# Kernel optimization log

Measured on AMD Instinct MI355X. Metric: run time of the kernel, lower is better.

The kernel has to match this reference:

```python
import jax, jax.numpy as jnp
import numpy as np

N, E, D, H, C = 20000, 320000, 256, 8, 32
NEG_SLOPE = 0.2


def setup_inputs() -> dict:
    key = jax.random.key(0)
    ks = jax.random.split(key, 9)
    s = 1.0 / np.sqrt(D)
    x = jax.random.normal(ks[0], (N, D), dtype=jnp.float32)
    edge_index = jax.random.randint(ks[1], (2, E), 0, N, dtype=jnp.int32)
    # positive edge weights in (0.05, 1.0] so log() is finite
    edge_attr = jax.random.uniform(ks[2], (E,), dtype=jnp.float32, minval=0.05, maxval=1.0)
    W_l = jax.random.normal(ks[3], (D, H * C), dtype=jnp.float32) * s
    b_l = jax.random.normal(ks[4], (H * C,), dtype=jnp.float32) * 0.01
    W_r = jax.random.normal(ks[5], (D, H * C), dtype=jnp.float32) * s
    b_r = jax.random.normal(ks[6], (H * C,), dtype=jnp.float32) * 0.01
    att = jax.random.normal(ks[7], (H, C), dtype=jnp.float32) * (1.0 / np.sqrt(C))
    bias = jax.random.normal(ks[8], (H * C,), dtype=jnp.float32) * 0.01
    return {"x": x, "edge_index": edge_index, "edge_attr": edge_attr,
            "W_l": W_l, "b_l": b_l, "W_r": W_r, "b_r": b_r,
            "att": att, "bias": bias}


def reference(x, edge_index, edge_attr, W_l, b_l, W_r, b_r, att, bias):
    n = x.shape[0]
    # GATv2: separate linear transforms for source (l) and target (r) nodes
    x_l = (x @ W_l + b_l).reshape(n, H, C)  # source / x_j
    x_r = (x @ W_r + b_r).reshape(n, H, C)  # target / x_i
    src, dst = edge_index[0], edge_index[1]  # flow: source_to_target, index = dst

    x_j = x_l[src]                            # [E, H, C]
    g = jax.nn.leaky_relu(x_r[dst] + x_j, NEG_SLOPE)
    alpha = jnp.einsum('ehc,hc->eh', g, att)  # [E, H]
    alpha = alpha + jnp.log(edge_attr)[:, None]

    # segment softmax over destination node (ragged edge groups)
    amax = jax.ops.segment_max(alpha, dst, num_segments=n)  # [N, H]
    ex = jnp.exp(alpha - amax[dst])
    denom = jax.ops.segment_sum(ex, dst, num_segments=n)
    alpha = ex / (denom[dst] + 1e-16)

    # message = x_j * alpha, scatter-add into destination nodes
    out = jax.ops.segment_sum(x_j * alpha[..., None], dst, num_segments=n)  # [N, H, C]
    return out.reshape(n, H * C) + bias
```

## Files before the change

### kernel.cpp

```cpp
#include <hip/hip_runtime.h>
#include <hip/hip_bf16.h>
#include <math.h>

#define DD 256
#define NHEAD 8
#define NEG_SLOPE 0.2f
#define CAP 64

typedef __attribute__((ext_vector_type(16))) float f32x16;
typedef __attribute__((ext_vector_type(8)))  short bf16x8;
typedef _Float16 h2 __attribute__((ext_vector_type(2)));

union Frag { bf16x8 v; uint4 u4; };
union HU4  { uint4 u4; h2 h[4]; };

__device__ inline uint f2bf(float f) {
    __hip_bfloat16 h = __float2bfloat16(f);
    return (uint)*(ushort*)&h;
}
__device__ inline ushort f2h(float f) {
    _Float16 h = (_Float16)f;
    return *(ushort*)&h;
}
__device__ inline h2 pkmax(h2 a, h2 b) {
    h2 d;
    asm("v_pk_max_f16 %0, %1, %2" : "=v"(d) : "v"(a), "v"(b));
    return d;
}
__device__ inline float hdot2(h2 a, h2 b, float c) {
#if __has_builtin(__builtin_amdgcn_fdot2)
    return __builtin_amdgcn_fdot2(a, b, c, false);
#else
    return c + (float)a.x * (float)b.x + (float)a.y * (float)b.y;
#endif
}

__global__ __launch_bounds__(256) void prep_kernel(const float* __restrict__ x,
                                                   const float* __restrict__ Wl,
                                                   const float* __restrict__ Wr,
                                                   ushort* __restrict__ pa,
                                                   ushort* __restrict__ pw,
                                                   int* __restrict__ counts,
                                                   int N, int Mpad) {
    int idx = blockIdx.x * 256 + threadIdx.x;
    if (idx < N) { counts[idx] = 0; return; }
    idx -= N;
    const int na = Mpad * 32;
    if (idx < na) {
        int lane = idx & 63;
        int mi   = (idx >> 6) & 1;
        int s16  = (idx >> 7) & 15;
        int tile = idx >> 11;
        int m = tile * 64 + mi * 32 + (lane & 31);
        int g = lane >> 5;
        uint4 val = {0u, 0u, 0u, 0u};
        if (m < N) {
            const float* xp = x + (size_t)m * DD + s16 * 16 + g * 4;
            float4 f0 = *(const float4*)xp;
            float4 f1 = *(const float4*)(xp + 8);
            val.x = f2bf(f0.x) | (f2bf(f0.y) << 16);
            val.y = f2bf(f0.z) | (f2bf(f0.w) << 16);
            val.z = f2bf(f1.x) | (f2bf(f1.y) << 16);
            val.w = f2bf(f1.z) | (f2bf(f1.w) << 16);
        }
        *(uint4*)(pa + (size_t)idx * 8) = val;
        return;
    }
    idx -= na;
    if (idx < 16384) {
        int lane = idx & 63;
        int s16  = (idx >> 6) & 15;
        int ng   = (idx >> 10) & 7;
        int mat  = idx >> 13;
        const float* W = mat ? Wr : Wl;
        int n  = ng * 32 + (lane & 31);
        int k0 = s16 * 16 + (lane >> 5) * 4;
        uint4 val;
        val.x = f2bf(W[(size_t)(k0 + 0) * DD + n]) | (f2bf(W[(size_t)(k0 + 1) * DD + n]) << 16);
        val.y = f2bf(W[(size_t)(k0 + 2) * DD + n]) | (f2bf(W[(size_t)(k0 + 3) * DD + n]) << 16);
        val.z = f2bf(W[(size_t)(k0 + 8) * DD + n]) | (f2bf(W[(size_t)(k0 + 9) * DD + n]) << 16);
        val.w = f2bf(W[(size_t)(k0 +10) * DD + n]) | (f2bf(W[(size_t)(k0 +11) * DD + n]) << 16);
        *(uint4*)(pw + (size_t)idx * 8) = val;
    }
}

__global__ __launch_bounds__(256) void scatter_kernel(const int* __restrict__ src,
                                                      const int* __restrict__ dst,
                                                      const float* __restrict__ w,
                                                      int* __restrict__ counts,
                                                      int2* __restrict__ csr_sw,
                                                      int E) {
    int e = blockIdx.x * 256 + threadIdx.x;
    if (e < E) {
        int d = dst[e];
        int pos = atomicAdd(&counts[d], 1);
        if (pos < CAP)
            csr_sw[((size_t)d << 6) + pos] = make_int2(src[e], __float_as_int(w[e]));
    }
}

__global__ __launch_bounds__(256, 4) void mm_kernel(const ushort* __restrict__ pa,
                                                    const ushort* __restrict__ pw,
                                                    const float* __restrict__ bl,
                                                    const float* __restrict__ br,
                                                    ushort* __restrict__ xl_h,
                                                    ushort* __restrict__ xr_h,
                                                    int N) {
    const int t    = threadIdx.x;
    const int lane = t & 63;
    const int l31  = lane & 31;
    const int g    = lane >> 5;
    const int wd   = t >> 6;
    const int tile = blockIdx.x, mat = blockIdx.y;

    const ushort* paT = pa + (size_t)tile * 2048 * 8;
    const ushort* pb  = pw + ((size_t)mat * 8192 + (size_t)(2 * wd) * 1024) * 8;

    f32x16 acc00, acc01, acc10, acc11;
    #pragma unroll
    for (int i = 0; i < 16; ++i) { acc00[i] = 0.f; acc01[i] = 0.f; acc10[i] = 0.f; acc11[i] = 0.f; }

    #pragma unroll 4
    for (int s16 = 0; s16 < 16; ++s16) {
        Frag a0, a1, b0, b1;
        a0.u4 = *(const uint4*)(paT + (size_t)((s16 * 2 + 0) * 64 + lane) * 8);
        a1.u4 = *(const uint4*)(paT + (size_t)((s16 * 2 + 1) * 64 + lane) * 8);
        b0.u4 = *(const uint4*)(pb  + (size_t)((s16     ) * 64 + lane) * 8);
        b1.u4 = *(const uint4*)(pb  + (size_t)((16 + s16) * 64 + lane) * 8);
        acc00 = __builtin_amdgcn_mfma_f32_32x32x16_bf16(a0.v, b0.v, acc00, 0, 0, 0);
        acc01 = __builtin_amdgcn_mfma_f32_32x32x16_bf16(a0.v, b1.v, acc01, 0, 0, 0);
        acc10 = __builtin_amdgcn_mfma_f32_32x32x16_bf16(a1.v, b0.v, acc10, 0, 0, 0);
        acc11 = __builtin_amdgcn_mfma_f32_32x32x16_bf16(a1.v, b1.v, acc11, 0, 0, 0);
    }

    const int n0 = wd * 64 + l31;
    const int n1 = n0 + 32;
    const float* bp = (mat == 0) ? bl : br;
    const float bv0 = bp[n0], bv1 = bp[n1];
    const int mb = tile * 64;
    ushort* dstp = (mat == 0) ? xl_h : xr_h;
    #pragma unroll
    for (int r = 0; r < 16; ++r) {
        int mloc = (r & 3) + 8 * (r >> 2) + 4 * g;
        int m0 = mb + mloc, m1 = m0 + 32;
        if (m0 < N) {
            dstp[(size_t)m0 * DD + n0] = f2h(acc00[r] + bv0);
            dstp[(size_t)m0 * DD + n1] = f2h(acc01[r] + bv1);
        }
        if (m1 < N) {
            dstp[(size_t)m1 * DD + n0] = f2h(acc10[r] + bv0);
            dstp[(size_t)m1 * DD + n1] = f2h(acc11[r] + bv1);
        }
    }
}

__global__ __launch_bounds__(256) void node_kernel(const int* __restrict__ counts,
                                                   const int2* __restrict__ csr_sw,
                                                   const ushort* __restrict__ xl_h,
                                                   const ushort* __restrict__ xr_h,
                                                   const float* __restrict__ att,
                                                   const float* __restrict__ bias,
                                                   float* __restrict__ out,
                                                   int N) {
    const int wid  = threadIdx.x >> 6;
    const int lane = threadIdx.x & 63;
    const int d = blockIdx.x * 4 + wid;
    if (d >= N) return;
    const int l31 = lane & 31;
    const int hi  = lane >> 5;
    const int c0  = l31 * 8;

    const size_t beg = (size_t)d << 6;
    const int deg = min(counts[d], CAP);

    HU4 xru; xru.u4 = *(const uint4*)(xr_h + (size_t)d * DD + c0);
    const float4 af0 = *(const float4*)(att + c0);
    const float4 af1 = *(const float4*)(att + c0 + 4);
    const h2 at0 = {(_Float16)af0.x, (_Float16)af0.y};
    const h2 at1 = {(_Float16)af0.z, (_Float16)af0.w};
    const h2 at2 = {(_Float16)af1.x, (_Float16)af1.y};
    const h2 at3 = {(_Float16)af1.z, (_Float16)af1.w};
    const h2 slope = {(_Float16)NEG_SLOPE, (_Float16)NEG_SLOPE};

    float dsum = 0.f;
    float ac[8];
    #pragma unroll
    for (int j = 0; j < 8; ++j) ac[j] = 0.f;

    auto body = [&](const HU4& xv, float we) {
        h2 a0 = xv.h[0] + xru.h[0];
        h2 a1 = xv.h[1] + xru.h[1];
        h2 a2 = xv.h[2] + xru.h[2];
        h2 a3 = xv.h[3] + xru.h[3];
        h2 g0 = pkmax(a0, a0 * slope);
        h2 g1 = pkmax(a1, a1 * slope);
        h2 g2 = pkmax(a2, a2 * slope);
        h2 g3 = pkmax(a3, a3 * slope);
        float p = hdot2(g3, at3, hdot2(g2, at2, hdot2(g1, at1, hdot2(g0, at0, 0.f))));
        p += __shfl_xor(p, 1);
        p += __shfl_xor(p, 2);
        float ev = we * __expf(p);
        dsum += ev;
        ac[0] += ev * (float)xv.h[0].x;
        ac[1] += ev * (float)xv.h[0].y;
        ac[2] += ev * (float)xv.h[1].x;
        ac[3] += ev * (float)xv.h[1].y;
        ac[4] += ev * (float)xv.h[2].x;
        ac[5] += ev * (float)xv.h[2].y;
        ac[6] += ev * (float)xv.h[3].x;
        ac[7] += ev * (float)xv.h[3].y;
    };

    const int npair = (deg + 1) >> 1;
    const int dm1   = deg - 1;
    int i = 0;
    for (; i + 2 <= npair; i += 2) {
        const int iA = 2 * i + hi;
        const int iB = iA + 2;
        int2 swA = csr_sw[beg + min(iA, dm1)];
        int2 swB = csr_sw[beg + min(iB, dm1)];
        float wA = (iA < deg) ? __int_as_float(swA.y) : 0.f;
        float wB = (iB < deg) ? __int_as_float(swB.y) : 0.f;
        HU4 xvA; xvA.u4 = *(const uint4*)(xl_h + (size_t)swA.x * DD + c0);
        HU4 xvB; xvB.u4 = *(const uint4*)(xl_h + (size_t)swB.x * DD + c0);
        body(xvA, wA);
        body(xvB, wB);
    }
    if (i < npair) {
        const int iA = 2 * i + hi;
        int2 swA = csr_sw[beg + min(iA, dm1)];
        float wA = (iA < deg) ? __int_as_float(swA.y) : 0.f;
        HU4 xvA; xvA.u4 = *(const uint4*)(xl_h + (size_t)swA.x * DD + c0);
        body(xvA, wA);
    }

    dsum += __shfl_xor(dsum, 32);
    #pragma unroll
    for (int j = 0; j < 8; ++j) ac[j] += __shfl_xor(ac[j], 32);
    const float inv = 1.f / (dsum + 1e-16f);

    const float4 bv = *(const float4*)(bias + c0 + 4 * hi);
    const int b = 4 * hi;
    float4 o;
    o.x = ac[b + 0] * inv + bv.x;
    o.y = ac[b + 1] * inv + bv.y;
    o.z = ac[b + 2] * inv + bv.z;
    o.w = ac[b + 3] * inv + bv.w;
    *(float4*)(out + (size_t)d * DD + c0 + 4 * hi) = o;
}

extern "C" void kernel_launch(void* const* d_in, const int* in_sizes, int n_in,
                              void* d_out, int out_size, void* d_ws, size_t ws_size,
                              hipStream_t stream) {
    const float* x    = (const float*)d_in[0];
    const int*   ei   = (const int*)  d_in[1];
    const float* w    = (const float*)d_in[2];
    const float* Wl   = (const float*)d_in[3];
    const float* bl   = (const float*)d_in[4];
    const float* Wr   = (const float*)d_in[5];
    const float* br   = (const float*)d_in[6];
    const float* att  = (const float*)d_in[7];
    const float* bias = (const float*)d_in[8];

    const int N = in_sizes[0] / DD;
    const int E = in_sizes[2];
    const int* src = ei;
    const int* dst = ei + E;

    const int Mtiles = (N + 63) / 64;
    const int Mpad   = Mtiles * 64;

    ushort* xr_h    = (ushort*)d_ws;
    ushort* xl_h    = xr_h + (size_t)N * DD;
    ushort* pa      = xl_h + (size_t)N * DD;
    ushort* pw      = pa + (size_t)Mpad * DD;
    int2*   csr_sw  = (int2*)(pw + 131072);
    int*    counts  = (int*)(csr_sw + (size_t)N * CAP);

    float* out = (float*)d_out;

    const int prep_total = N + Mpad * 32 + 16384;
    prep_kernel   <<<(prep_total + 255) / 256, 256, 0, stream>>>(x, Wl, Wr,
                                                                 pa, pw, counts,
                                                                 N, Mpad);
    scatter_kernel<<<(E + 255) / 256, 256, 0, stream>>>(src, dst, w, counts,
                                                        csr_sw, E);
    mm_kernel     <<<dim3(Mtiles, 2), 256, 0, stream>>>(pa, pw, bl, br,
                                                        xl_h, xr_h, N);
    node_kernel   <<<(N + 3) / 4, 256, 0, stream>>>(counts, csr_sw,
                                                    xl_h, xr_h, att, bias, out, N);
}
```

Before: 77.19 us.

## Fuse x bf16 conversion into matmul, use fp16 accumulators, unroll gather by four

Removes the packed-A staging pass from the prep kernel: the matmul now reads fp32 rows of x directly and converts them to bf16 in registers before the MFMA. This drops a full write and reread of the packed activation buffer, but each of the two matrix blocks now reads x in fp32. The node kernel keeps its weighted feature sums in packed fp16 and unrolls the edge gather loop by four, putting more loads in flight. The fp16 accumulation risks precision loss and overflow on high-degree nodes.

```diff
diff --git a/kernel.cpp b/kernel.cpp
--- a/kernel.cpp
+++ b/kernel.cpp
@@ -34,39 +34,23 @@
     return c + (float)a.x * (float)b.x + (float)a.y * (float)b.y;
 #endif
 }
-
-__global__ __launch_bounds__(256) void prep_kernel(const float* __restrict__ x,
-                                                   const float* __restrict__ Wl,
+__device__ inline uint4 pack8bf(float4 lo, float4 hi) {
+    uint4 v;
+    v.x = f2bf(lo.x) | (f2bf(lo.y) << 16);
+    v.y = f2bf(lo.z) | (f2bf(lo.w) << 16);
+    v.z = f2bf(hi.x) | (f2bf(hi.y) << 16);
+    v.w = f2bf(hi.z) | (f2bf(hi.w) << 16);
+    return v;
+}
+
+__global__ __launch_bounds__(256) void prep_kernel(const float* __restrict__ Wl,
                                                    const float* __restrict__ Wr,
-                                                   ushort* __restrict__ pa,
                                                    ushort* __restrict__ pw,
                                                    int* __restrict__ counts,
-                                                   int N, int Mpad) {
+                                                   int N) {
     int idx = blockIdx.x * 256 + threadIdx.x;
     if (idx < N) { counts[idx] = 0; return; }
     idx -= N;
-    const int na = Mpad * 32;
-    if (idx < na) {
-        int lane = idx & 63;
-        int mi   = (idx >> 6) & 1;
-        int s16  = (idx >> 7) & 15;
-        int tile = idx >> 11;
-        int m = tile * 64 + mi * 32 + (lane & 31);
-        int g = lane >> 5;
-        uint4 val = {0u, 0u, 0u, 0u};
-        if (m < N) {
-            const float* xp = x + (size_t)m * DD + s16 * 16 + g * 4;
-            float4 f0 = *(const float4*)xp;
-            float4 f1 = *(const float4*)(xp + 8);
-            val.x = f2bf(f0.x) | (f2bf(f0.y) << 16);
-            val.y = f2bf(f0.z) | (f2bf(f0.w) << 16);
-            val.z = f2bf(f1.x) | (f2bf(f1.y) << 16);
-            val.w = f2bf(f1.z) | (f2bf(f1.w) << 16);
-        }
-        *(uint4*)(pa + (size_t)idx * 8) = val;
-        return;
-    }
-    idx -= na;
     if (idx < 16384) {
         int lane = idx & 63;
         int s16  = (idx >> 6) & 15;
@@ -99,7 +83,7 @@
     }
 }
 
-__global__ __launch_bounds__(256, 4) void mm_kernel(const ushort* __restrict__ pa,
+__global__ __launch_bounds__(256, 4) void mm_kernel(const float* __restrict__ x,
                                                     const ushort* __restrict__ pw,
                                                     const float* __restrict__ bl,
                                                     const float* __restrict__ br,
@@ -112,9 +96,11 @@
     const int g    = lane >> 5;
     const int wd   = t >> 6;
     const int tile = blockIdx.x, mat = blockIdx.y;
-
-    const ushort* paT = pa + (size_t)tile * 2048 * 8;
-    const ushort* pb  = pw + ((size_t)mat * 8192 + (size_t)(2 * wd) * 1024) * 8;
+    const int mb   = tile * 64;
+
+    const float* xrow0 = x + (size_t)min(mb + l31,      N - 1) * DD;
+    const float* xrow1 = x + (size_t)min(mb + 32 + l31, N - 1) * DD;
+    const ushort* pb   = pw + ((size_t)mat * 8192 + (size_t)(2 * wd) * 1024) * 8;
 
     f32x16 acc00, acc01, acc10, acc11;
     #pragma unroll
@@ -122,11 +108,16 @@
 
     #pragma unroll 4
     for (int s16 = 0; s16 < 16; ++s16) {
+        const int off = s16 * 16 + g * 4;
         Frag a0, a1, b0, b1;
-        a0.u4 = *(const uint4*)(paT + (size_t)((s16 * 2 + 0) * 64 + lane) * 8);
-        a1.u4 = *(const uint4*)(paT + (size_t)((s16 * 2 + 1) * 64 + lane) * 8);
-        b0.u4 = *(const uint4*)(pb  + (size_t)((s16     ) * 64 + lane) * 8);
-        b1.u4 = *(const uint4*)(pb  + (size_t)((16 + s16) * 64 + lane) * 8);
+        float4 lo0 = *(const float4*)(xrow0 + off);
+        float4 hi0 = *(const float4*)(xrow0 + off + 8);
+        float4 lo1 = *(const float4*)(xrow1 + off);
+        float4 hi1 = *(const float4*)(xrow1 + off + 8);
+        b0.u4 = *(const uint4*)(pb + (size_t)((s16     ) * 64 + lane) * 8);
+        b1.u4 = *(const uint4*)(pb + (size_t)((16 + s16) * 64 + lane) * 8);
+        a0.u4 = pack8bf(lo0, hi0);
+        a1.u4 = pack8bf(lo1, hi1);
         acc00 = __builtin_amdgcn_mfma_f32_32x32x16_bf16(a0.v, b0.v, acc00, 0, 0, 0);
         acc01 = __builtin_amdgcn_mfma_f32_32x32x16_bf16(a0.v, b1.v, acc01, 0, 0, 0);
         acc10 = __builtin_amdgcn_mfma_f32_32x32x16_bf16(a1.v, b0.v, acc10, 0, 0, 0);
@@ -137,7 +128,6 @@
     const int n1 = n0 + 32;
     const float* bp = (mat == 0) ? bl : br;
     const float bv0 = bp[n0], bv1 = bp[n1];
-    const int mb = tile * 64;
     ushort* dstp = (mat == 0) ? xl_h : xr_h;
     #pragma unroll
     for (int r = 0; r < 16; ++r) {
@@ -183,9 +173,9 @@
     const h2 slope = {(_Float16)NEG_SLOPE, (_Float16)NEG_SLOPE};
 
     float dsum = 0.f;
-    float ac[8];
-    #pragma unroll
-    for (int j = 0; j < 8; ++j) ac[j] = 0.f;
+    h2 ac2[4];
+    #pragma unroll
+    for (int j = 0; j < 4; ++j) ac2[j] = (h2){(_Float16)0.f, (_Float16)0.f};
 
     auto body = [&](const HU4& xv, float we) {
         h2 a0 = xv.h[0] + xru.h[0];
@@ -201,32 +191,38 @@
         p += __shfl_xor(p, 2);
         float ev = we * __expf(p);
         dsum += ev;
-        ac[0] += ev * (float)xv.h[0].x;
-        ac[1] += ev * (float)xv.h[0].y;
-        ac[2] += ev * (float)xv.h[1].x;
-        ac[3] += ev * (float)xv.h[1].y;
-        ac[4] += ev * (float)xv.h[2].x;
-        ac[5] += ev * (float)xv.h[2].y;
-        ac[6] += ev * (float)xv.h[3].x;
-        ac[7] += ev * (float)xv.h[3].y;
+        _Float16 evh = (_Float16)ev;
+        h2 evv = {evh, evh};
+        ac2[0] += evv * xv.h[0];
+        ac2[1] += evv * xv.h[1];
+        ac2[2] += evv * xv.h[2];
+        ac2[3] += evv * xv.h[3];
     };
 
     const int npair = (deg + 1) >> 1;
     const int dm1   = deg - 1;
     int i = 0;
-    for (; i + 2 <= npair; i += 2) {
+    for (; i + 4 <= npair; i += 4) {
         const int iA = 2 * i + hi;
-        const int iB = iA + 2;
+        const int iB = iA + 2, iC = iA + 4, iD = iA + 6;
         int2 swA = csr_sw[beg + min(iA, dm1)];
         int2 swB = csr_sw[beg + min(iB, dm1)];
+        int2 swC = csr_sw[beg + min(iC, dm1)];
+        int2 swD = csr_sw[beg + min(iD, dm1)];
         float wA = (iA < deg) ? __int_as_float(swA.y) : 0.f;
         float wB = (iB < deg) ? __int_as_float(swB.y) : 0.f;
+        float wC = (iC < deg) ? __int_as_float(swC.y) : 0.f;
+        float wD = (iD < deg) ? __int_as_float(swD.y) : 0.f;
         HU4 xvA; xvA.u4 = *(const uint4*)(xl_h + (size_t)swA.x * DD + c0);
         HU4 xvB; xvB.u4 = *(const uint4*)(xl_h + (size_t)swB.x * DD + c0);
+        HU4 xvC; xvC.u4 = *(const uint4*)(xl_h + (size_t)swC.x * DD + c0);
+        HU4 xvD; xvD.u4 = *(const uint4*)(xl_h + (size_t)swD.x * DD + c0);
         body(xvA, wA);
         body(xvB, wB);
-    }
-    if (i < npair) {
+        body(xvC, wC);
+        body(xvD, wD);
+    }
+    for (; i < npair; ++i) {
         const int iA = 2 * i + hi;
         int2 swA = csr_sw[beg + min(iA, dm1)];
         float wA = (iA < deg) ? __int_as_float(swA.y) : 0.f;
@@ -234,6 +230,12 @@
         body(xvA, wA);
     }
 
+    float ac[8];
+    #pragma unroll
+    for (int j = 0; j < 4; ++j) {
+        ac[2 * j]     = (float)ac2[j].x;
+        ac[2 * j + 1] = (float)ac2[j].y;
+    }
     dsum += __shfl_xor(dsum, 32);
     #pragma unroll
     for (int j = 0; j < 8; ++j) ac[j] += __shfl_xor(ac[j], 32);
@@ -268,24 +270,21 @@
     const int* dst = ei + E;
 
     const int Mtiles = (N + 63) / 64;
-    const int Mpad   = Mtiles * 64;
 
     ushort* xr_h    = (ushort*)d_ws;
     ushort* xl_h    = xr_h + (size_t)N * DD;
-    ushort* pa      = xl_h + (size_t)N * DD;
-    ushort* pw      = pa + (size_t)Mpad * DD;
+    ushort* pw      = xl_h + (size_t)N * DD;
     int2*   csr_sw  = (int2*)(pw + 131072);
     int*    counts  = (int*)(csr_sw + (size_t)N * CAP);
 
     float* out = (float*)d_out;
 
-    const int prep_total = N + Mpad * 32 + 16384;
-    prep_kernel   <<<(prep_total + 255) / 256, 256, 0, stream>>>(x, Wl, Wr,
-                                                                 pa, pw, counts,
-                                                                 N, Mpad);
+    const int prep_total = N + 16384;
+    prep_kernel   <<<(prep_total + 255) / 256, 256, 0, stream>>>(Wl, Wr, pw,
+                                                                 counts, N);
     scatter_kernel<<<(E + 255) / 256, 256, 0, stream>>>(src, dst, w, counts,
                                                         csr_sw, E);
-    mm_kernel     <<<dim3(Mtiles, 2), 256, 0, stream>>>(pa, pw, bl, br,
+    mm_kernel     <<<dim3(Mtiles, 2), 256, 0, stream>>>(x, pw, bl, br,
                                                         xl_h, xr_h, N);
     node_kernel   <<<(N + 3) / 4, 256, 0, stream>>>(counts, csr_sw,
                                                     xl_h, xr_h, att, bias, out, N);
```

Measured after the change: 88.93 us. 1.15x slower.
